# Kernel optimization log

Hardware: AMD Instinct MI355X
Metric: run time of the kernel (lower is better)

Reference implementation:

```python
import jax, jax.numpy as jnp
import numpy as np

B, S, E, NH = 2, 2048, 1024, 8
DH = E // NH


def setup_inputs() -> dict:
    key = jax.random.key(0)
    ks = jax.random.split(key, 8)
    q = jax.random.normal(ks[0], (B, S, E), dtype=jnp.float32)
    k = jax.random.normal(ks[1], (B, S, E), dtype=jnp.float32)
    v = jax.random.normal(ks[2], (B, S, E), dtype=jnp.float32)
    # gate projections: Linear(3E -> NH)
    igate_w = jax.random.normal(ks[3], (NH, 3 * E), dtype=jnp.float32) * 0.02
    igate_b = jax.random.normal(ks[4], (NH,), dtype=jnp.float32) * 0.1
    fgate_w = jax.random.normal(ks[5], (NH, 3 * E), dtype=jnp.float32) * 0.02
    fgate_b = jnp.linspace(3.0, 6.0, NH, dtype=jnp.float32)  # bias_linspace_init_
    norm_weight = 1.0 + 0.01 * jax.random.normal(ks[6], (E,), dtype=jnp.float32)
    return {"q": q, "k": k, "v": v, "igate_w": igate_w, "igate_b": igate_b,
            "fgate_w": fgate_w, "fgate_b": fgate_b, "norm_weight": norm_weight}


def _mlstm_forward(q, k, v, igate_w, igate_b, fgate_w, fgate_b, norm_weight):
    eps = 1e-6
    gate_in = jnp.concatenate([q, k, v], axis=-1)            # (B,S,3E)
    i_pre = gate_in @ igate_w.T + igate_b                    # (B,S,NH)
    f_pre = gate_in @ fgate_w.T + fgate_b                    # (B,S,NH)
    i_pre = jnp.transpose(i_pre, (0, 2, 1))                  # (B,NH,S)
    f_pre = jnp.transpose(f_pre, (0, 2, 1))                  # (B,NH,S)

    qh = jnp.transpose(q.reshape(B, S, NH, DH), (0, 2, 1, 3))  # (B,NH,S,DH)
    kh = jnp.transpose(k.reshape(B, S, NH, DH), (0, 2, 1, 3))
    vh = jnp.transpose(v.reshape(B, S, NH, DH), (0, 2, 1, 3))

    # cumulative log forget gates; decay matrix D[i,j] = sum_{u=j+1..i} logsig(f_u) + i_pre[j]
    log_fg = jax.nn.log_sigmoid(f_pre)                       # (B,NH,S)
    cs = jnp.cumsum(log_fg, axis=-1)                         # (B,NH,S)
    diff = cs[:, :, :, None] - cs[:, :, None, :]             # (B,NH,S,S) = cs[i]-cs[j]
    causal = jnp.tril(jnp.ones((S, S), dtype=bool))
    log_fg_mat = jnp.where(causal, diff, -jnp.inf)
    log_D = log_fg_mat + i_pre[:, :, None, :]                # (B,NH,S,S)

    max_log_D = jnp.max(log_D, axis=-1, keepdims=True)       # rowwise stabilizer
    D = jnp.exp(log_D - max_log_D)

    qk = jnp.einsum("bhsd,bhtd->bhst", qh, kh / jnp.sqrt(jnp.float32(DH)))
    C = qk * D
    normalizer = jnp.maximum(jnp.abs(jnp.sum(C, axis=-1, keepdims=True)),
                             jnp.exp(-max_log_D))
    Cn = C / (normalizer + eps)
    h = jnp.einsum("bhst,bhtd->bhsd", Cn, vh)                # (B,NH,S,DH)

    # MultiHeadLayerNorm == group_norm(num_groups=NH): per-head, per-token over DH
    mu = jnp.mean(h, axis=-1, keepdims=True)
    var = jnp.var(h, axis=-1, keepdims=True)
    hn = (h - mu) / jnp.sqrt(var + 1e-5)
    hn = hn * norm_weight.reshape(NH, DH)[None, :, None, :]
    return jnp.transpose(hn, (0, 2, 1, 3)).reshape(B, S, E)


def reference(q, k, v, igate_w, igate_b, fgate_w, fgate_b, norm_weight):
    return _mlstm_forward(q, k, v, igate_w, igate_b, fgate_w, fgate_b, norm_weight)
```

## Files before the change

### kernel.cpp

```cpp
#include <hip/hip_runtime.h>
#include <hip/hip_bf16.h>
#include <math.h>

typedef __attribute__((ext_vector_type(8))) short bf16x8;
typedef __attribute__((ext_vector_type(16))) float f32x16;

namespace {
constexpr int kB = 2, kS = 2048, kE = 1024, kNH = 8, kDH = 128, kE3 = 3072;
constexpr float kLog2e = 1.4426950408889634f;
constexpr int kUnits = 27;
constexpr int kSplitPerBh = 20;
}

__device__ const int kOrder[kUnits] = {6,19,20,17,18,5,15,16,13,14,24,25,4,
                                       11,12,21,22,23,26,9,10,3,7,8,2,1,0};

__device__ __forceinline__ ushort f2bf(float x) {
  union { __hip_bfloat16 b; ushort u; } c; c.b = __float2bfloat16(x); return c.u;
}
__device__ __forceinline__ uint pk2(float a, float b) {
  return (uint)f2bf(a) | ((uint)f2bf(b) << 16);
}
__device__ __forceinline__ void gload16(const void* g, void* l) {
  __builtin_amdgcn_global_load_lds(
      (const __attribute__((address_space(1))) void*)g,
      (__attribute__((address_space(3))) void*)l, 16, 0, 0);
}
__device__ __forceinline__ f32x16 zero16() {
  f32x16 z;
#pragma unroll
  for (int i = 0; i < 16; ++i) z[i] = 0.f;
  return z;
}
union UB8 { uint4 u; bf16x8 f; };

__device__ __forceinline__ float butterfly64(float* acc, int lane) {
  int cur = 64;
#pragma unroll
  for (int lv = 0; lv < 6; ++lv) {
    const int bmask = 1 << lv;
    const int half = cur >> 1;
    const bool hi = (lane & bmask) != 0;
#pragma unroll
    for (int i = 0; i < 32; ++i) {
      if (i >= half) break;
      const float keep = hi ? acc[i + half] : acc[i];
      const float send = hi ? acc[i] : acc[i + half];
      acc[i] = keep + __shfl_xor(send, bmask);
    }
    cur = half;
  }
  return acc[0];
}

__global__ __launch_bounds__(256) void preproc_kernel(
    const float* __restrict__ q, const float* __restrict__ k, const float* __restrict__ v,
    const float* __restrict__ iw, const float* __restrict__ ib,
    const float* __restrict__ fw, const float* __restrict__ fb,
    ushort* __restrict__ Kb, ushort* __restrict__ Vtb,
    float* __restrict__ i_pre, float* __restrict__ f_pre) {
  const int b = blockIdx.y;
  const int s0 = blockIdx.x * 8;
  const int tid = threadIdx.x;
  const int w = tid >> 6, lane = tid & 63;
  __shared__ ushort Vst[8 * 1024];

#pragma unroll
  for (int t = 0; t < 2; ++t) {
    const int tokl = w * 2 + t;
    const int s = s0 + tokl;
    const size_t base = ((size_t)b * kS + s) * kE + lane * 16;
    const int hh = lane >> 3;

    const float4 k0 = *reinterpret_cast<const float4*>(k + base);
    const float4 k1 = *reinterpret_cast<const float4*>(k + base + 4);
    const float4 k2 = *reinterpret_cast<const float4*>(k + base + 8);
    const float4 k3 = *reinterpret_cast<const float4*>(k + base + 12);
    uint4 pa, pb;
    pa.x = pk2(k0.x, k0.y); pa.y = pk2(k0.z, k0.w);
    pa.z = pk2(k1.x, k1.y); pa.w = pk2(k1.z, k1.w);
    pb.x = pk2(k2.x, k2.y); pb.y = pk2(k2.z, k2.w);
    pb.z = pk2(k3.x, k3.y); pb.w = pk2(k3.z, k3.w);
    ushort* kd = Kb + ((size_t)(b * 8 + hh) * kS + s) * 128 + (lane & 7) * 16;
    *reinterpret_cast<uint4*>(kd) = pa;
    *reinterpret_cast<uint4*>(kd + 8) = pb;

    const float4 v0 = *reinterpret_cast<const float4*>(v + base);
    const float4 v1 = *reinterpret_cast<const float4*>(v + base + 4);
    const float4 v2 = *reinterpret_cast<const float4*>(v + base + 8);
    const float4 v3 = *reinterpret_cast<const float4*>(v + base + 12);
    uint4 va, vb4;
    va.x = pk2(v0.x, v0.y); va.y = pk2(v0.z, v0.w);
    va.z = pk2(v1.x, v1.y); va.w = pk2(v1.z, v1.w);
    vb4.x = pk2(v2.x, v2.y); vb4.y = pk2(v2.z, v2.w);
    vb4.z = pk2(v3.x, v3.y); vb4.w = pk2(v3.z, v3.w);
    const int cc0 = lane * 2, cc1 = lane * 2 + 1;
    *reinterpret_cast<uint4*>(reinterpret_cast<char*>(Vst) + tokl * 2048 +
                              ((cc0 ^ ((cc0 >> 3) & 7)) << 4)) = va;
    *reinterpret_cast<uint4*>(reinterpret_cast<char*>(Vst) + tokl * 2048 +
                              ((cc1 ^ ((cc1 >> 3) & 7)) << 4)) = vb4;
  }
  __syncthreads();

#pragma unroll
  for (int j = 0; j < 4; ++j) {
    const int e = j * 256 + tid;
    const int cc = e >> 3;
    const int off = ((cc ^ ((cc >> 3) & 7)) << 4) + (e & 7) * 2;
    uint tmp[4];
#pragma unroll
    for (int t2 = 0; t2 < 8; t2 += 2) {
      const ushort u0 = *reinterpret_cast<const ushort*>(
          reinterpret_cast<const char*>(Vst) + t2 * 2048 + off);
      const ushort u1 = *reinterpret_cast<const ushort*>(
          reinterpret_cast<const char*>(Vst) + (t2 + 1) * 2048 + off);
      tmp[t2 >> 1] = (uint)u0 | ((uint)u1 << 16);
    }
    uint4 o; o.x = tmp[0]; o.y = tmp[1]; o.z = tmp[2]; o.w = tmp[3];
    ushort* vd = Vtb + ((size_t)(b * 8 + (e >> 7)) * 128 + (e & 127)) * kS + s0;
    *reinterpret_cast<uint4*>(vd) = o;
  }
  __syncthreads();

  const int kh = w >> 1, gh = w & 1;
  const float* __restrict__ W = gh ? fw : iw;
  float acc[64];
#pragma unroll
  for (int i = 0; i < 64; ++i) acc[i] = 0.f;

  for (int step = 0; step < 24; ++step) {
    const int e = kh * 1536 + step * 64 + lane;
    const int seg = e >> 10;
    const int eo = e & 1023;
    const float* __restrict__ src = (seg == 0) ? q : (seg == 1) ? k : v;
    float gv[8];
#pragma unroll
    for (int t = 0; t < 8; ++t)
      gv[t] = src[((size_t)b * kS + s0 + t) * kE + eo];
    float w8[8];
#pragma unroll
    for (int hh = 0; hh < 8; ++hh) w8[hh] = W[hh * kE3 + e];
#pragma unroll
    for (int t = 0; t < 8; ++t)
#pragma unroll
      for (int hh = 0; hh < 8; ++hh)
        acc[t * 8 + hh] += gv[t] * w8[hh];
  }
  const float r = butterfly64(acc, lane);
  const int a = ((lane & 1) << 5) | ((lane & 2) << 3) | ((lane & 4) << 1) |
                ((lane & 8) >> 1) | ((lane & 16) >> 3) | ((lane & 32) >> 5);
  float* red = reinterpret_cast<float*>(Vst);
  red[w * 64 + a] = r;
  __syncthreads();
  if (tid < 128) {
    const int t = tid >> 4, g16 = tid & 15, hh = g16 & 7;
    const float val = (g16 < 8) ? red[0 * 64 + t * 8 + hh] + red[2 * 64 + t * 8 + hh]
                                : red[1 * 64 + t * 8 + hh] + red[3 * 64 + t * 8 + hh];
    const size_t idx = ((size_t)(b * 8 + hh)) * kS + s0 + t;
    if (g16 < 8) i_pre[idx] = val + ib[hh];
    else         f_pre[idx] = val + fb[hh];
  }
}

__global__ __launch_bounds__(256) void scan_kernel(
    const float* __restrict__ i_pre, const float* __restrict__ f_pre,
    float* __restrict__ wt_out, float* __restrict__ M2_out, float* __restrict__ nfl_out,
    float* __restrict__ Cg) {
  const int bh = blockIdx.x;
  const int tid = threadIdx.x;
  const int w = tid >> 6, lane = tid & 63;
  __shared__ float wsum[4], wmax[4];
  const float* __restrict__ fp = f_pre + (size_t)bh * kS;
  const float* __restrict__ ip = i_pre + (size_t)bh * kS;
  const int s0 = tid * 8;

  const float4 fa = *reinterpret_cast<const float4*>(fp + s0);
  const float4 fb4 = *reinterpret_cast<const float4*>(fp + s0 + 4);
  float lf[8];
  {
    const float fv[8] = {fa.x, fa.y, fa.z, fa.w, fb4.x, fb4.y, fb4.z, fb4.w};
#pragma unroll
    for (int j = 0; j < 8; ++j)
      lf[j] = fminf(fv[j], 0.f) - log1pf(expf(-fabsf(fv[j])));
  }
  float run = 0.f, pcs[8];
#pragma unroll
  for (int j = 0; j < 8; ++j) { run += lf[j]; pcs[j] = run; }
  float x = run;
#pragma unroll
  for (int d = 1; d < 64; d <<= 1) {
    const float t = __shfl_up(x, d);
    if (lane >= d) x += t;
  }
  if (lane == 63) wsum[w] = x;
  __syncthreads();
  float woff = 0.f;
#pragma unroll
  for (int i = 0; i < 4; ++i) if (i < w) woff += wsum[i];
  const float csbase = woff + x - run;
  float cs[8];
#pragma unroll
  for (int j = 0; j < 8; ++j) cs[j] = csbase + pcs[j];

  const float4 ia = *reinterpret_cast<const float4*>(ip + s0);
  const float4 ib4 = *reinterpret_cast<const float4*>(ip + s0 + 4);
  float av[8];
  {
    const float iv[8] = {ia.x, ia.y, ia.z, ia.w, ib4.x, ib4.y, ib4.z, ib4.w};
#pragma unroll
    for (int j = 0; j < 8; ++j) av[j] = iv[j] - cs[j];
  }
  float rmax = -1e30f, pm[8];
#pragma unroll
  for (int j = 0; j < 8; ++j) { rmax = fmaxf(rmax, av[j]); pm[j] = rmax; }

  float tm = rmax;
  tm = fmaxf(tm, __shfl_xor(tm, 1));
  tm = fmaxf(tm, __shfl_xor(tm, 2));
  tm = fmaxf(tm, __shfl_xor(tm, 4));
  if ((lane & 7) == 0) Cg[bh * 32 + (tid >> 3)] = tm * kLog2e;

  float4 wtlo, wthi;
  wtlo.x = exp2f((av[0] - tm) * kLog2e); wtlo.y = exp2f((av[1] - tm) * kLog2e);
  wtlo.z = exp2f((av[2] - tm) * kLog2e); wtlo.w = exp2f((av[3] - tm) * kLog2e);
  wthi.x = exp2f((av[4] - tm) * kLog2e); wthi.y = exp2f((av[5] - tm) * kLog2e);
  wthi.z = exp2f((av[6] - tm) * kLog2e); wthi.w = exp2f((av[7] - tm) * kLog2e);

  float mi = rmax;
#pragma unroll
  for (int d = 1; d < 64; d <<= 1) {
    const float t = __shfl_up(mi, d);
    if (lane >= d) mi = fmaxf(mi, t);
  }
  if (lane == 63) wmax[w] = mi;
  float mexcl = __shfl_up(mi, 1);
  if (lane == 0) mexcl = -1e30f;
  __syncthreads();
  float wmoff = -1e30f;
#pragma unroll
  for (int i = 0; i < 4; ++i) if (i < w) wmoff = fmaxf(wmoff, wmax[i]);
  const float mbase = fmaxf(wmoff, mexcl);

  float M[8];
#pragma unroll
  for (int j = 0; j < 8; ++j) M[j] = fmaxf(mbase, pm[j]);
  float4 m2lo, m2hi, nflo, nfhi;
  m2lo.x = M[0] * kLog2e; m2lo.y = M[1] * kLog2e; m2lo.z = M[2] * kLog2e; m2lo.w = M[3] * kLog2e;
  m2hi.x = M[4] * kLog2e; m2hi.y = M[5] * kLog2e; m2hi.z = M[6] * kLog2e; m2hi.w = M[7] * kLog2e;
  nflo.x = expf(-(cs[0] + M[0])); nflo.y = expf(-(cs[1] + M[1]));
  nflo.z = expf(-(cs[2] + M[2])); nflo.w = expf(-(cs[3] + M[3]));
  nfhi.x = expf(-(cs[4] + M[4])); nfhi.y = expf(-(cs[5] + M[5]));
  nfhi.z = expf(-(cs[6] + M[6])); nfhi.w = expf(-(cs[7] + M[7]));
  const size_t o = (size_t)bh * kS + s0;
  *reinterpret_cast<float4*>(wt_out + o) = wtlo;
  *reinterpret_cast<float4*>(wt_out + o + 4) = wthi;
  *reinterpret_cast<float4*>(M2_out + o) = m2lo;
  *reinterpret_cast<float4*>(M2_out + o + 4) = m2hi;
  *reinterpret_cast<float4*>(nfl_out + o) = nflo;
  *reinterpret_cast<float4*>(nfl_out + o + 4) = nfhi;
}

__global__ __launch_bounds__(256, 2) void attn_mfma_kernel(
    const float* __restrict__ qg, const ushort* __restrict__ Kb,
    const ushort* __restrict__ Vtb, const float* __restrict__ wt,
    const float* __restrict__ Cg, const float* __restrict__ M2,
    const float* __restrict__ nfl, const float* __restrict__ nw,
    float* __restrict__ out, float* __restrict__ ph, float* __restrict__ prs) {
  const int id = blockIdx.x;
  const int r8 = id & 7, qq = id >> 3;
  const int bh = r8 + 8 * (qq & 1);
  const int u = kOrder[qq >> 1];
  const int b = bh >> 3, h = bh & 7;
  int it, j0, j1, cid = -1;
  if (u <= 6) { it = u; const int T = 2 * it + 2; j0 = 0; j1 = T - 1; }
  else if (u <= 20) {
    const int s = u - 7; it = 7 + (s >> 1); const int ci = s & 1;
    const int T = 2 * it + 2;
    j0 = (T * ci) >> 1; j1 = ((T * (ci + 1)) >> 1) - 1;
    cid = bh * kSplitPerBh + (u - 7);
  } else {
    const int s = u - 21; it = 14 + (s >= 3 ? 1 : 0); const int ci = s - (s >= 3 ? 3 : 0);
    const int T = 2 * it + 2;
    j0 = (T * ci) / 3; j1 = (T * (ci + 1)) / 3 - 1;
    cid = bh * kSplitPerBh + (u - 7);
  }
  const int tid = threadIdx.x;
  const int w = tid >> 6, lane = tid & 63;
  const int l31 = lane & 31, hi = lane >> 5;
  const int row_w = it * 128 + w * 32;
  const int ig = row_w + l31;
  const size_t bhS = (size_t)bh * kS;

  __shared__ ushort Klds[2 * 64 * 128];
  __shared__ ushort Vlds[2 * 128 * 64];

  const char* __restrict__ KgBase = reinterpret_cast<const char*>(Kb + bhS * 128);
  const char* __restrict__ VgBase = reinterpret_cast<const char*>(Vtb + (size_t)bh * 128 * kS);
  const float* __restrict__ wtb = wt + bhS;

  bf16x8 qf[8];
  {
    const float scale = 0.08838834764831845f;
    const float* qrow = qg + ((size_t)b * kS + ig) * kE + h * kDH;
#pragma unroll
    for (int ks = 0; ks < 8; ++ks) {
      const int d0 = ks * 16 + hi * 8;
      const float4 lo = *reinterpret_cast<const float4*>(qrow + d0);
      const float4 hi4 = *reinterpret_cast<const float4*>(qrow + d0 + 4);
      UB8 f;
      f.u.x = pk2(lo.x * scale, lo.y * scale);
      f.u.y = pk2(lo.z * scale, lo.w * scale);
      f.u.z = pk2(hi4.x * scale, hi4.y * scale);
      f.u.w = pk2(hi4.z * scale, hi4.w * scale);
      qf[ks] = f.f;
    }
  }
  const float M2i = M2[bhS + ig];
  const float cgreg = Cg[bh * 32 + l31];

  int koffG[4], voffG[4];
#pragma unroll
  for (int i = 0; i < 4; ++i) {
    const int L = tid * 16 + i * 4096;
    { const int j = L >> 8, c = (L >> 4) & 15;
      koffG[i] = j * 256 + ((c ^ (j & 15)) << 4); }
    { const int d = L >> 7, c = (L >> 4) & 7;
      voffG[i] = d * 4096 + ((c ^ (d & 7)) << 4); }
  }
  auto stage = [&](int buf, int jt) {
    const char* Kg = KgBase + (size_t)jt * 16384;
    const char* Vg = VgBase + (size_t)jt * 128;
    char* kl = reinterpret_cast<char*>(Klds) + buf * 16384 + tid * 16;
    char* vl = reinterpret_cast<char*>(Vlds) + buf * 16384 + tid * 16;
#pragma unroll
    for (int i = 0; i < 4; ++i) gload16(Kg + koffG[i], kl + i * 4096);
#pragma unroll
    for (int i = 0; i < 4; ++i) gload16(Vg + voffG[i], vl + i * 4096);
  };

  f32x16 hacc[4];
#pragma unroll
  for (int dc = 0; dc < 4; ++dc) hacc[dc] = zero16();
  float rs = 0.f;

  float wtc0 = wtb[j0 * 64 + l31];
  float wtc1 = wtb[j0 * 64 + 32 + l31];
  stage(0, j0);
  __syncthreads();

  for (int jt = j0; jt <= j1; ++jt) {
    const int cur = (jt - j0) & 1;
    float wtn0, wtn1;
    if (jt < j1) {
      stage(cur ^ 1, jt + 1);
      wtn0 = wtb[(jt + 1) * 64 + l31];
      wtn1 = wtb[(jt + 1) * 64 + 32 + l31];
    }
    const int jlo = jt * 64;
    const bool v0 = (jlo <= row_w + 31);
    const bool v1 = (jlo + 32 <= row_w + 31);
    const bool fullmask = (jlo + 63 <= row_w);

    if (v0) {
      const float f = exp2f(__shfl(cgreg, jt) - M2i);
      const char* kb = reinterpret_cast<const char*>(Klds) + cur * 16384;
      const char* vb = reinterpret_cast<const char*>(Vlds) + cur * 16384;
      const int ksw = (l31 & 15) << 4;

      f32x16 sacc0 = zero16(), sacc1 = zero16();
#pragma unroll
      for (int ks = 0; ks < 8; ++ks) {
        const int colb = 32 * ks + 16 * hi;
        const bf16x8 kf0 = *reinterpret_cast<const bf16x8*>(
            kb + l31 * 256 + (colb ^ ksw));
        sacc0 = __builtin_amdgcn_mfma_f32_32x32x16_bf16(kf0, qf[ks], sacc0, 0, 0, 0);
        if (v1) {
          const bf16x8 kf1 = *reinterpret_cast<const bf16x8*>(
              kb + (32 + l31) * 256 + (colb ^ ksw));
          sacc1 = __builtin_amdgcn_mfma_f32_32x32x16_bf16(kf1, qf[ks], sacc1, 0, 0, 0);
        }
      }

      uint pkw[2][8];
#pragma unroll
      for (int jc = 0; jc < 2; ++jc) {
        if (jc == 1 && !v1) break;
        const f32x16 sa = jc ? sacc1 : sacc0;
        float p[16];
#pragma unroll
        for (int r = 0; r < 16; ++r) {
          const int c = (r & 3) + 8 * (r >> 2);
          const float wv = __shfl(jc ? wtc1 : wtc0, c + 4 * hi);
          float val = sa[r] * (wv * f);
          if (!fullmask) val = (jlo + jc * 32 + c + 4 * hi <= ig) ? val : 0.f;
          rs += val; p[r] = val;
        }
#pragma unroll
        for (int q2 = 0; q2 < 8; ++q2) pkw[jc][q2] = pk2(p[2 * q2], p[2 * q2 + 1]);
      }

#pragma unroll
      for (int ks = 0; ks < 4; ++ks) {
        const int jc = ks >> 1, ks2 = ks & 1;
        if (jc == 1 && !v1) break;
        UB8 pf;
        pf.u.x = pkw[jc][ks2 * 4 + 0]; pf.u.y = pkw[jc][ks2 * 4 + 1];
        pf.u.z = pkw[jc][ks2 * 4 + 2]; pf.u.w = pkw[jc][ks2 * 4 + 3];
        const int colb = 64 * jc + 32 * ks2 + 8 * hi;
#pragma unroll
        for (int dc = 0; dc < 4; ++dc) {
          const int d = dc * 32 + l31;
          const char* vrow = vb + d * 128;
          const int sw = (d & 7) << 4;
          const uint2 a = *reinterpret_cast<const uint2*>(vrow + (colb ^ sw));
          const uint2 c = *reinterpret_cast<const uint2*>(vrow + ((colb + 16) ^ sw));
          UB8 vf; vf.u.x = a.x; vf.u.y = a.y; vf.u.z = c.x; vf.u.w = c.y;
          hacc[dc] = __builtin_amdgcn_mfma_f32_32x32x16_bf16(pf.f, vf.f, hacc[dc], 0, 0, 0);
        }
      }
    }
    __syncthreads();
    if (jt < j1) { wtc0 = wtn0; wtc1 = wtn1; }
  }

  const float rs_tot = rs + __shfl_xor(rs, 32);

  if (cid >= 0) {
    float* pb = ph + (size_t)cid * 16384;
#pragma unroll
    for (int dc = 0; dc < 4; ++dc)
#pragma unroll
      for (int r = 0; r < 16; ++r) {
        const int il = w * 32 + (r & 3) + 8 * (r >> 2) + 4 * hi;
        pb[il * 128 + dc * 32 + l31] = hacc[dc][r];
      }
    if (hi == 0) prs[cid * 128 + w * 32 + l31] = rs_tot;
    return;
  }

  float nwv[4];
#pragma unroll
  for (int dc = 0; dc < 4; ++dc) nwv[dc] = nw[h * kDH + dc * 32 + l31];
#pragma unroll
  for (int r = 0; r < 16; ++r) {
    const int imap = (r & 3) + 8 * (r >> 2) + 4 * hi;
    const float rsum = __shfl(rs_tot, imap);
    const float nf = nfl[bhS + row_w + imap];
    const float inv = 1.f / (fmaxf(fabsf(rsum), nf) + 1e-6f);
    float hv[4];
    float s1 = 0.f, s2 = 0.f;
#pragma unroll
    for (int dc = 0; dc < 4; ++dc) {
      hv[dc] = hacc[dc][r] * inv;
      s1 += hv[dc]; s2 += hv[dc] * hv[dc];
    }
#pragma unroll
    for (int off = 1; off <= 16; off <<= 1) {
      s1 += __shfl_xor(s1, off);
      s2 += __shfl_xor(s2, off);
    }
    const float mu = s1 * (1.f / 128.f);
    const float var = s2 * (1.f / 128.f) - mu * mu;
    const float rstd = rsqrtf(var + 1e-5f);
    float* __restrict__ orow = out + ((size_t)b * kS + row_w + imap) * kE + h * kDH;
#pragma unroll
    for (int dc = 0; dc < 4; ++dc)
      orow[dc * 32 + l31] = (hv[dc] - mu) * rstd * nwv[dc];
  }
}

__global__ __launch_bounds__(256) void combine_kernel(
    const float* __restrict__ ph, const float* __restrict__ prs,
    const float* __restrict__ nfl, const float* __restrict__ nw,
    float* __restrict__ out) {
  const int blk = blockIdx.x;
  const int bh = blk / 9, ct = blk % 9;
  const int b = bh >> 3, h = bh & 7;
  const int it = 7 + ct;
  const int nc = (ct < 7) ? 2 : 3;
  const int cb0 = bh * kSplitPerBh + ((ct < 7) ? ct * 2 : 14 + (ct - 7) * 3);
  const int tid = threadIdx.x;
  __shared__ float sinv[128];
  if (tid < 128) {
    float rsum = 0.f;
    for (int c = 0; c < nc; ++c) rsum += prs[(cb0 + c) * 128 + tid];
    const float nf = nfl[(size_t)bh * kS + it * 128 + tid];
    sinv[tid] = 1.f / (fmaxf(fabsf(rsum), nf) + 1e-6f);
  }
  __syncthreads();
  for (int kk = 0; kk < 16; ++kk) {
    const int idx = kk * 256 + tid;
    const int row = idx >> 5, c4 = idx & 31;
    float ax = 0.f, ay = 0.f, az = 0.f, aw = 0.f;
    for (int c = 0; c < nc; ++c) {
      const float4 t = *reinterpret_cast<const float4*>(
          ph + (size_t)(cb0 + c) * 16384 + row * 128 + c4 * 4);
      ax += t.x; ay += t.y; az += t.z; aw += t.w;
    }
    const float inv = sinv[row];
    ax *= inv; ay *= inv; az *= inv; aw *= inv;
    float s1 = ax + ay + az + aw;
    float s2 = ax * ax + ay * ay + az * az + aw * aw;
#pragma unroll
    for (int off = 1; off <= 16; off <<= 1) {
      s1 += __shfl_xor(s1, off);
      s2 += __shfl_xor(s2, off);
    }
    const float mu = s1 * (1.f / 128.f);
    const float var = s2 * (1.f / 128.f) - mu * mu;
    const float rstd = rsqrtf(var + 1e-5f);
    const float4 nw4 = *reinterpret_cast<const float4*>(nw + h * kDH + c4 * 4);
    float4 o;
    o.x = (ax - mu) * rstd * nw4.x;
    o.y = (ay - mu) * rstd * nw4.y;
    o.z = (az - mu) * rstd * nw4.z;
    o.w = (aw - mu) * rstd * nw4.w;
    *reinterpret_cast<float4*>(
        out + ((size_t)b * kS + it * 128 + row) * kE + h * kDH + c4 * 4) = o;
  }
}

extern "C" void kernel_launch(void* const* d_in, const int* in_sizes, int n_in,
                              void* d_out, int out_size, void* d_ws, size_t ws_size,
                              hipStream_t stream) {
  const float* q  = (const float*)d_in[0];
  const float* k  = (const float*)d_in[1];
  const float* v  = (const float*)d_in[2];
  const float* iw = (const float*)d_in[3];
  const float* ib = (const float*)d_in[4];
  const float* fw = (const float*)d_in[5];
  const float* fb = (const float*)d_in[6];
  const float* nw = (const float*)d_in[7];
  float* out = (float*)d_out;

  char* ws = (char*)d_ws;
  const int BHS = kB * kNH * kS;
  float* i_pre = (float*)ws;
  float* f_pre = i_pre + BHS;
  float* wt    = i_pre + 2 * BHS;
  float* M2    = i_pre + 3 * BHS;
  float* nfl   = i_pre + 4 * BHS;
  float* Cg    = i_pre + 5 * BHS;
  ushort* Kb  = (ushort*)(ws + (size_t)(5 * BHS + 512) * 4);
  ushort* Vtb = Kb + (size_t)kB * kNH * kS * kDH;
  float* ph   = (float*)(Vtb + (size_t)kB * kNH * kS * kDH);
  float* prs  = ph + (size_t)320 * 128 * 128;

  preproc_kernel<<<dim3(kS / 8, kB), dim3(256), 0, stream>>>(
      q, k, v, iw, ib, fw, fb, Kb, Vtb, i_pre, f_pre);
  scan_kernel<<<dim3(kB * kNH), dim3(256), 0, stream>>>(i_pre, f_pre, wt, M2, nfl, Cg);
  attn_mfma_kernel<<<dim3(kUnits * kB * kNH), dim3(256), 0, stream>>>(
      q, Kb, Vtb, wt, Cg, M2, nfl, nw, out, ph, prs);
  combine_kernel<<<dim3(kB * kNH * 9), dim3(256), 0, stream>>>(ph, prs, nfl, nw, out);
}
```

Measured before the change: 122.6 us.

## Split preprocessing into separate K/V conversion and gate projection kernels

The fused preprocessing kernel is split in two. One kernel converts K/V to bf16 per (batch, head) tile of 32 tokens, with a wider V transpose through swizzled shared memory. The other computes both input and forget gate projections for 4 tokens per block, with each warp covering a quarter of the 3E reduction. The aim is more blocks, less serialized work per block and better coalescing of the V-transpose stores. The cost is an extra kernel launch and re-reading K and V from global memory in two kernels.

```diff
diff --git a/kernel.cpp b/kernel.cpp
--- a/kernel.cpp
+++ b/kernel.cpp
@@ -53,25 +53,20 @@
   return acc[0];
 }
 
-__global__ __launch_bounds__(256) void preproc_kernel(
-    const float* __restrict__ q, const float* __restrict__ k, const float* __restrict__ v,
-    const float* __restrict__ iw, const float* __restrict__ ib,
-    const float* __restrict__ fw, const float* __restrict__ fb,
-    ushort* __restrict__ Kb, ushort* __restrict__ Vtb,
-    float* __restrict__ i_pre, float* __restrict__ f_pre) {
-  const int b = blockIdx.y;
-  const int s0 = blockIdx.x * 8;
+__global__ __launch_bounds__(256) void convkv_kernel(
+    const float* __restrict__ k, const float* __restrict__ v,
+    ushort* __restrict__ Kb, ushort* __restrict__ Vtb) {
+  const int bh = blockIdx.y;
+  const int b = bh >> 3, h = bh & 7;
+  const int s0 = blockIdx.x * 32;
   const int tid = threadIdx.x;
-  const int w = tid >> 6, lane = tid & 63;
-  __shared__ ushort Vst[8 * 1024];
-
-#pragma unroll
-  for (int t = 0; t < 2; ++t) {
-    const int tokl = w * 2 + t;
-    const int s = s0 + tokl;
-    const size_t base = ((size_t)b * kS + s) * kE + lane * 16;
-    const int hh = lane >> 3;
-
+  __shared__ ushort Vst[32 * 128];
+
+  const int tl = tid >> 3;
+  const int d0 = (tid & 7) * 16;
+  const int s = s0 + tl;
+  {
+    const size_t base = ((size_t)b * kS + s) * kE + h * kDH + d0;
     const float4 k0 = *reinterpret_cast<const float4*>(k + base);
     const float4 k1 = *reinterpret_cast<const float4*>(k + base + 4);
     const float4 k2 = *reinterpret_cast<const float4*>(k + base + 8);
@@ -81,7 +76,7 @@
     pa.z = pk2(k1.x, k1.y); pa.w = pk2(k1.z, k1.w);
     pb.x = pk2(k2.x, k2.y); pb.y = pk2(k2.z, k2.w);
     pb.z = pk2(k3.x, k3.y); pb.w = pk2(k3.z, k3.w);
-    ushort* kd = Kb + ((size_t)(b * 8 + hh) * kS + s) * 128 + (lane & 7) * 16;
+    ushort* kd = Kb + ((size_t)bh * kS + s) * 128 + d0;
     *reinterpret_cast<uint4*>(kd) = pa;
     *reinterpret_cast<uint4*>(kd + 8) = pb;
 
@@ -94,71 +89,86 @@
     va.z = pk2(v1.x, v1.y); va.w = pk2(v1.z, v1.w);
     vb4.x = pk2(v2.x, v2.y); vb4.y = pk2(v2.z, v2.w);
     vb4.z = pk2(v3.x, v3.y); vb4.w = pk2(v3.z, v3.w);
-    const int cc0 = lane * 2, cc1 = lane * 2 + 1;
-    *reinterpret_cast<uint4*>(reinterpret_cast<char*>(Vst) + tokl * 2048 +
-                              ((cc0 ^ ((cc0 >> 3) & 7)) << 4)) = va;
-    *reinterpret_cast<uint4*>(reinterpret_cast<char*>(Vst) + tokl * 2048 +
-                              ((cc1 ^ ((cc1 >> 3) & 7)) << 4)) = vb4;
+    const int c0 = d0 >> 3;
+    char* row = reinterpret_cast<char*>(Vst) + tl * 256;
+    *reinterpret_cast<uint4*>(row + (((c0 + 0) ^ (tl & 15)) << 4)) = va;
+    *reinterpret_cast<uint4*>(row + (((c0 + 1) ^ (tl & 15)) << 4)) = vb4;
   }
   __syncthreads();
 
-#pragma unroll
-  for (int j = 0; j < 4; ++j) {
-    const int e = j * 256 + tid;
-    const int cc = e >> 3;
-    const int off = ((cc ^ ((cc >> 3) & 7)) << 4) + (e & 7) * 2;
-    uint tmp[4];
-#pragma unroll
-    for (int t2 = 0; t2 < 8; t2 += 2) {
+  {
+    const int d = tid >> 1, half = tid & 1;
+    const int cd = d >> 3;
+    const int od = (d & 7) * 2;
+    uint tmp[8];
+#pragma unroll
+    for (int p = 0; p < 8; ++p) {
+      const int t = half * 16 + 2 * p;
       const ushort u0 = *reinterpret_cast<const ushort*>(
-          reinterpret_cast<const char*>(Vst) + t2 * 2048 + off);
+          reinterpret_cast<const char*>(Vst) + t * 256 + ((cd ^ (t & 15)) << 4) + od);
       const ushort u1 = *reinterpret_cast<const ushort*>(
-          reinterpret_cast<const char*>(Vst) + (t2 + 1) * 2048 + off);
-      tmp[t2 >> 1] = (uint)u0 | ((uint)u1 << 16);
-    }
-    uint4 o; o.x = tmp[0]; o.y = tmp[1]; o.z = tmp[2]; o.w = tmp[3];
-    ushort* vd = Vtb + ((size_t)(b * 8 + (e >> 7)) * 128 + (e & 127)) * kS + s0;
-    *reinterpret_cast<uint4*>(vd) = o;
-  }
-  __syncthreads();
-
-  const int kh = w >> 1, gh = w & 1;
-  const float* __restrict__ W = gh ? fw : iw;
+          reinterpret_cast<const char*>(Vst) + (t + 1) * 256 + ((cd ^ ((t + 1) & 15)) << 4) + od);
+      tmp[p] = (uint)u0 | ((uint)u1 << 16);
+    }
+    ushort* vd = Vtb + ((size_t)bh * kDH + d) * kS + s0 + half * 16;
+    uint4 o0, o1;
+    o0.x = tmp[0]; o0.y = tmp[1]; o0.z = tmp[2]; o0.w = tmp[3];
+    o1.x = tmp[4]; o1.y = tmp[5]; o1.z = tmp[6]; o1.w = tmp[7];
+    *reinterpret_cast<uint4*>(vd) = o0;
+    *reinterpret_cast<uint4*>(vd + 8) = o1;
+  }
+}
+
+__global__ __launch_bounds__(256) void gates_kernel(
+    const float* __restrict__ q, const float* __restrict__ k, const float* __restrict__ v,
+    const float* __restrict__ iw, const float* __restrict__ ib,
+    const float* __restrict__ fw, const float* __restrict__ fb,
+    float* __restrict__ i_pre, float* __restrict__ f_pre) {
+  const int tid = threadIdx.x;
+  const int w = tid >> 6, lane = tid & 63;
+  const int tokbase = blockIdx.x * 4;
   float acc[64];
 #pragma unroll
   for (int i = 0; i < 64; ++i) acc[i] = 0.f;
 
-  for (int step = 0; step < 24; ++step) {
-    const int e = kh * 1536 + step * 64 + lane;
+  for (int step = 0; step < 12; ++step) {
+    const int e = w * 768 + step * 64 + lane;
     const int seg = e >> 10;
     const int eo = e & 1023;
     const float* __restrict__ src = (seg == 0) ? q : (seg == 1) ? k : v;
-    float gv[8];
-#pragma unroll
-    for (int t = 0; t < 8; ++t)
-      gv[t] = src[((size_t)b * kS + s0 + t) * kE + eo];
-    float w8[8];
-#pragma unroll
-    for (int hh = 0; hh < 8; ++hh) w8[hh] = W[hh * kE3 + e];
-#pragma unroll
-    for (int t = 0; t < 8; ++t)
-#pragma unroll
-      for (int hh = 0; hh < 8; ++hh)
-        acc[t * 8 + hh] += gv[t] * w8[hh];
+    float gv[4];
+#pragma unroll
+    for (int t = 0; t < 4; ++t)
+      gv[t] = src[(size_t)(tokbase + t) * kE + eo];
+    float wi[8], wf[8];
+#pragma unroll
+    for (int hh = 0; hh < 8; ++hh) {
+      wi[hh] = iw[hh * kE3 + e];
+      wf[hh] = fw[hh * kE3 + e];
+    }
+#pragma unroll
+    for (int t = 0; t < 4; ++t) {
+#pragma unroll
+      for (int hh = 0; hh < 8; ++hh) {
+        acc[t * 16 + hh]     += gv[t] * wi[hh];
+        acc[t * 16 + 8 + hh] += gv[t] * wf[hh];
+      }
+    }
   }
   const float r = butterfly64(acc, lane);
   const int a = ((lane & 1) << 5) | ((lane & 2) << 3) | ((lane & 4) << 1) |
                 ((lane & 8) >> 1) | ((lane & 16) >> 3) | ((lane & 32) >> 5);
-  float* red = reinterpret_cast<float*>(Vst);
-  red[w * 64 + a] = r;
+  __shared__ float red[4][64];
+  red[w][a] = r;
   __syncthreads();
-  if (tid < 128) {
-    const int t = tid >> 4, g16 = tid & 15, hh = g16 & 7;
-    const float val = (g16 < 8) ? red[0 * 64 + t * 8 + hh] + red[2 * 64 + t * 8 + hh]
-                                : red[1 * 64 + t * 8 + hh] + red[3 * 64 + t * 8 + hh];
-    const size_t idx = ((size_t)(b * 8 + hh)) * kS + s0 + t;
-    if (g16 < 8) i_pre[idx] = val + ib[hh];
-    else         f_pre[idx] = val + fb[hh];
+  if (tid < 64) {
+    const float val = red[0][tid] + red[1][tid] + red[2][tid] + red[3][tid];
+    const int t = tid >> 4, gate = tid & 15, hh = gate & 7;
+    const int token = tokbase + t;
+    const int b = token >> 11, s = token & 2047;
+    const size_t idx = ((size_t)(b * 8 + hh)) * kS + s;
+    if (gate < 8) i_pre[idx] = val + ib[hh];
+    else          f_pre[idx] = val + fb[hh];
   }
 }
 
@@ -546,8 +556,9 @@
   float* ph   = (float*)(Vtb + (size_t)kB * kNH * kS * kDH);
   float* prs  = ph + (size_t)320 * 128 * 128;
 
-  preproc_kernel<<<dim3(kS / 8, kB), dim3(256), 0, stream>>>(
-      q, k, v, iw, ib, fw, fb, Kb, Vtb, i_pre, f_pre);
+  convkv_kernel<<<dim3(kS / 32, kB * kNH), dim3(256), 0, stream>>>(k, v, Kb, Vtb);
+  gates_kernel<<<dim3(kB * kS / 4), dim3(256), 0, stream>>>(q, k, v, iw, ib, fw, fb,
+                                                            i_pre, f_pre);
   scan_kernel<<<dim3(kB * kNH), dim3(256), 0, stream>>>(i_pre, f_pre, wt, M2, nfl, Cg);
   attn_mfma_kernel<<<dim3(kUnits * kB * kNH), dim3(256), 0, stream>>>(
       q, Kb, Vtb, wt, Cg, M2, nfl, nw, out, ph, prs);
```

Result: no change. 123.0 us (+0.3%).
